# Kernel optimization log

Hardware: AMD Instinct MI355X
Metric: run time of the kernel (lower is better)

The kernel has to match this reference:

```python
import jax, jax.numpy as jnp
import numpy as np

B, T, C, H = 8, 4096, 384, 64

def setup_inputs() -> dict:
    key = jax.random.key(0)
    k1, k2, k3, k4 = jax.random.split(key, 4)
    x = jax.random.normal(k1, (B, T, C), dtype=jnp.float32)
    # nn.Linear(C, H, bias=False) weight applied as x @ W (W stored [C, H])
    s = 1.0 / np.sqrt(C)
    Wk = jax.random.normal(k2, (C, H), dtype=jnp.float32) * s
    Wq = jax.random.normal(k3, (C, H), dtype=jnp.float32) * s
    Wv = jax.random.normal(k4, (C, H), dtype=jnp.float32) * s
    return {"x": x, "Wk": Wk, "Wq": Wq, "Wv": Wv}

def reference(x, Wk, Wq, Wv):
    Bx, Tx, Cx = x.shape
    k = x @ Wk  # [B,T,H]
    q = x @ Wq  # [B,T,H]
    v = x @ Wv  # [B,T,H]
    # NOTE: original scales by C**-0.5 (embedding dim), not head_size**-0.5
    w = jnp.einsum('bth,bsh->bts', q, k) * (Cx ** -0.5)  # [B,T,T]
    causal = jnp.tril(jnp.ones((Tx, Tx), dtype=bool))
    w = jnp.where(causal, w, -jnp.inf)
    w = jax.nn.softmax(w, axis=-1)
    # dropout omitted (eval mode / deterministic reference)
    out = jnp.einsum('bts,bsh->bth', w, v)  # [B,T,H]
    return out
```

## Files before the change

### kernel.cpp

```cpp
#include <hip/hip_runtime.h>
#include <hip/hip_bf16.h>


typedef __bf16 bf16x8 __attribute__((ext_vector_type(8)));
typedef float  f32x4  __attribute__((ext_vector_type(4)));

#define BB   8
#define TT   4096
#define CC   384
#define HH   64
#define NROW (BB*TT)
#define QSCALE (0.05103103630798288f * 1.4426950408889634f)

#if __has_builtin(__builtin_amdgcn_exp2f)
#define EXP2(x) __builtin_amdgcn_exp2f(x)
#else
#define EXP2(x) exp2f(x)
#endif

#define LDS_ROUNDTRIP_FENCE() __asm volatile("s_waitcnt lgkmcnt(0)" ::: "memory")

__device__ __forceinline__ unsigned short f2bf(float f) {
    __bf16 h = (__bf16)f;
    return __builtin_bit_cast(unsigned short, h);
}

__global__ __launch_bounds__(256) void wtrans_kernel(
        const float* __restrict__ Wk,
        const float* __restrict__ Wq,
        const float* __restrict__ Wv,
        unsigned short* __restrict__ Wt) {
    __shared__ __align__(16) unsigned short tile[64][72];
    const float* Wm = (blockIdx.y == 0) ? Wk : ((blockIdx.y == 1) ? Wq : Wv);
    unsigned short* Wtm = Wt + blockIdx.y * (HH * CC);
    const int c0 = blockIdx.x * 64;
#pragma unroll
    for (int i = 0; i < 16; ++i) {
        int id = threadIdx.x + i * 256;
        int c = id >> 6, h = id & 63;
        tile[c][h] = f2bf(Wm[(c0 + c) * HH + h]);
    }
    __syncthreads();
#pragma unroll
    for (int i = 0; i < 16; ++i) {
        int id = threadIdx.x + i * 256;
        int h = id >> 6, c = id & 63;
        Wtm[h * CC + c0 + c] = tile[c][h];
    }
}

__global__ __launch_bounds__(512) void qkv_kernel(
        const float* __restrict__ x,
        const unsigned short* __restrict__ Wt,
        unsigned short* __restrict__ q_ws,
        unsigned short* __restrict__ k_ws,
        unsigned short* __restrict__ vt_ws) {
    __shared__ __align__(16) f32x4 xacc[256 * 13];
    __shared__ __align__(16) unsigned short vtile[64][72];

    const int lane = threadIdx.x & 63;
    const int wv8  = threadIdx.x >> 6;
    const int grp  = wv8 >> 2;
    const int wg   = wv8 & 3;
    const int g256 = threadIdx.x & 255;
    const int l15  = lane & 15;
    const int quad = lane >> 4;
    const int rb   = blockIdx.x * 64;
    const int row  = rb + wg * 16 + l15;

    f32x4 acc[3][4];
    const f32x4 zero = {0.f, 0.f, 0.f, 0.f};
#pragma unroll
    for (int m = 0; m < 3; ++m)
#pragma unroll
        for (int nt = 0; nt < 4; ++nt) acc[m][nt] = zero;

    const float* xrow = x + (long)row * CC + grp * 192;
#pragma unroll
    for (int ch = 0; ch < 3; ++ch) {
#pragma unroll
        for (int kg = 0; kg < 2; ++kg) {
            const int coff = ch * 64 + kg * 32 + quad * 8;
            float4 u0 = *reinterpret_cast<const float4*>(xrow + coff);
            float4 u1 = *reinterpret_cast<const float4*>(xrow + coff + 4);
            bf16x8 a;
            a[0] = (__bf16)u0.x; a[1] = (__bf16)u0.y;
            a[2] = (__bf16)u0.z; a[3] = (__bf16)u0.w;
            a[4] = (__bf16)u1.x; a[5] = (__bf16)u1.y;
            a[6] = (__bf16)u1.z; a[7] = (__bf16)u1.w;
            const int gcoff = grp * 192 + coff;
#pragma unroll
            for (int m = 0; m < 3; ++m) {
                const unsigned short* wtm = Wt + m * (HH * CC);
#pragma unroll
                for (int nt = 0; nt < 4; ++nt) {
                    bf16x8 bfr = *reinterpret_cast<const bf16x8*>(
                        wtm + (nt * 16 + l15) * CC + gcoff);
                    acc[m][nt] = __builtin_amdgcn_mfma_f32_16x16x32_bf16(
                        a, bfr, acc[m][nt], 0, 0, 0);
                }
            }
        }
    }

    const int cidx = g256 * 13;
    if (grp == 1) {
#pragma unroll
        for (int m = 0; m < 3; ++m)
#pragma unroll
            for (int nt = 0; nt < 4; ++nt)
                xacc[cidx + m * 4 + nt] = acc[m][nt];
    }
    __syncthreads();

    if (grp == 0) {
#pragma unroll
        for (int m = 0; m < 3; ++m)
#pragma unroll
            for (int nt = 0; nt < 4; ++nt)
                acc[m][nt] += xacc[cidx + m * 4 + nt];

        const int rt = (rb >> 4) + wg;
#pragma unroll
        for (int nt = 0; nt < 4; ++nt) {
            const int h  = nt * 16 + l15;
            const int c8 = h >> 3;
            const int jj = h & 7;
#pragma unroll
            for (int r = 0; r < 4; ++r) {
                const int gr = rb + wg * 16 + quad * 4 + r;
                const int ii = quad * 4 + r;
                k_ws[((rt * 8 + c8) * 16 + ii) * 8 + jj] = f2bf(acc[0][nt][r]);
                q_ws[gr * HH + h] = f2bf(acc[1][nt][r] * QSCALE);
                vtile[h][ii + wg * 16] = f2bf(acc[2][nt][r]);
            }
        }
    }
    __syncthreads();
    {
        int id = threadIdx.x;
        int dt = id >> 7, sc = (id >> 4) & 7, ii = id & 15;
        unsigned short* dst = vt_ws + (long)(rb >> 6) * 4096
                              + (dt * 8 + sc) * 128 + ii * 8;
        *reinterpret_cast<uint4*>(dst) =
            *reinterpret_cast<const uint4*>(&vtile[dt * 16 + ii][sc * 8]);
    }
}

__global__ __launch_bounds__(1024, 4) void attn_kernel(
        const unsigned short* __restrict__ q_ws,
        const unsigned short* __restrict__ k_ws,
        const unsigned short* __restrict__ vt_ws,
        float* __restrict__ out) {
    __shared__ __align__(16) unsigned short P_lds[16 * 16 * 64];
    __shared__ __align__(16) float xchg[64 * 65];
    __shared__ float mx1[64], lx1[64];

    const int lane = threadIdx.x & 63;
    const int wv16 = threadIdx.x >> 6;
    const int grp  = wv16 >> 2;
    const int wg   = wv16 & 3;
    const int l15  = lane & 15;
    const int quad = lane >> 4;

    const int bid = blockIdx.x;
    const int b   = bid & 7;
    const int qt  = (TT / 64 - 1) - (bid >> 3);
    const int qrow = qt * 64 + wg * 16 + l15;

    const unsigned short* qbase = q_ws + (b * TT + qrow) * HH;
    const bf16x8 qf0 = *reinterpret_cast<const bf16x8*>(qbase + quad * 8);
    const bf16x8 qf1 = *reinterpret_cast<const bf16x8*>(qbase + 32 + quad * 8);

    const f32x4 zero = {0.f, 0.f, 0.f, 0.f};
    f32x4 o[4];
#pragma unroll
    for (int dt = 0; dt < 4; ++dt) o[dt] = zero;
    float mprev = -1e30f, lsum = 0.f;

    const int pbase = wv16 * 1024 + l15 * 64;
    const int pxor  = (l15 & 7) << 3;

    for (int t = grp; t <= qt; t += 4) {
        const int s0 = t * 64;
        const unsigned short* ktile = k_ws + ((long)((b * TT + s0) >> 4)) * 1024;
        const unsigned short* vtile = vt_ws + ((long)((b * TT + s0) >> 6)) * 4096;

        bf16x8 ka0[4], ka1[4];
#pragma unroll
        for (int st = 0; st < 4; ++st) {
            ka0[st] = *reinterpret_cast<const bf16x8*>(
                ktile + ((st * 8 + quad) * 16 + l15) * 8);
            ka1[st] = *reinterpret_cast<const bf16x8*>(
                ktile + ((st * 8 + 4 + quad) * 16 + l15) * 8);
        }
        bf16x8 vb0[4], vb1[4];
#pragma unroll
        for (int dt = 0; dt < 4; ++dt) {
            vb0[dt] = *reinterpret_cast<const bf16x8*>(
                vtile + dt * 1024 + quad * 128 + l15 * 8);
            vb1[dt] = *reinterpret_cast<const bf16x8*>(
                vtile + dt * 1024 + (4 + quad) * 128 + l15 * 8);
        }

        f32x4 sc[4];
#pragma unroll
        for (int st = 0; st < 4; ++st) {
            f32x4 z = zero;
            z = __builtin_amdgcn_mfma_f32_16x16x32_bf16(ka0[st], qf0, z, 0, 0, 0);
            z = __builtin_amdgcn_mfma_f32_16x16x32_bf16(ka1[st], qf1, z, 0, 0, 0);
            sc[st] = z;
        }

        if (t == qt) {
#pragma unroll
            for (int st = 0; st < 4; ++st)
#pragma unroll
                for (int r = 0; r < 4; ++r) {
                    int sg = s0 + st * 16 + quad * 4 + r;
                    if (sg > qrow) sc[st][r] = -1e30f;
                }
        }

        float mloc = -1e30f;
#pragma unroll
        for (int st = 0; st < 4; ++st)
#pragma unroll
            for (int r = 0; r < 4; ++r) mloc = fmaxf(mloc, sc[st][r]);
        mloc = fmaxf(mloc, __shfl_xor(mloc, 16));
        mloc = fmaxf(mloc, __shfl_xor(mloc, 32));
        const float mnew = fmaxf(mprev, mloc);
        const unsigned long long anych = __ballot(mnew > mprev);
        float alpha = 1.0f;
        if (anych) alpha = EXP2(mprev - mnew);

        float psum = 0.f;
#pragma unroll
        for (int st = 0; st < 4; ++st) {
            union { unsigned short us[4]; uint2 u2; } pk;
#pragma unroll
            for (int r = 0; r < 4; ++r) {
                float p = EXP2(sc[st][r] - mnew);
                psum += p;
                pk.us[r] = f2bf(p);
            }
            *reinterpret_cast<uint2*>(
                &P_lds[pbase + ((st * 16 + quad * 4) ^ pxor)]) = pk.u2;
        }
        psum += __shfl_xor(psum, 16);
        psum += __shfl_xor(psum, 32);
        lsum = lsum * alpha + psum;
        mprev = mnew;

        if (anych) {
            float ar[4];
#pragma unroll
            for (int r = 0; r < 4; ++r) ar[r] = __shfl(alpha, quad * 4 + r);
#pragma unroll
            for (int dt = 0; dt < 4; ++dt)
#pragma unroll
                for (int r = 0; r < 4; ++r) o[dt][r] *= ar[r];
        }

        LDS_ROUNDTRIP_FENCE();

        bf16x8 pf0 = *reinterpret_cast<const bf16x8*>(
            &P_lds[pbase + ((quad * 8) ^ pxor)]);
        bf16x8 pf1 = *reinterpret_cast<const bf16x8*>(
            &P_lds[pbase + ((32 + quad * 8) ^ pxor)]);
#pragma unroll
        for (int dt = 0; dt < 4; ++dt) {
            o[dt] = __builtin_amdgcn_mfma_f32_16x16x32_bf16(pf0, vb0[dt], o[dt], 0, 0, 0);
            o[dt] = __builtin_amdgcn_mfma_f32_16x16x32_bf16(pf1, vb1[dt], o[dt], 0, 0, 0);
        }
    }

    for (int rr = 1; rr < 4; ++rr) {
        __syncthreads();
        if (grp == rr) {
            if (quad == 0) { mx1[wg * 16 + l15] = mprev; lx1[wg * 16 + l15] = lsum; }
#pragma unroll
            for (int dt = 0; dt < 4; ++dt)
#pragma unroll
                for (int r = 0; r < 4; ++r)
                    xchg[(wg * 16 + quad * 4 + r) * 65 + dt * 16 + l15] = o[dt][r];
        }
        __syncthreads();
        if (grp == 0) {
#pragma unroll
            for (int r = 0; r < 4; ++r) {
                const int row = wg * 16 + quad * 4 + r;
                const float m0r = __shfl(mprev, quad * 4 + r);
                const float m1r = mx1[row];
                const float ms  = fmaxf(m0r, m1r);
                const float w0  = EXP2(m0r - ms);
                const float w1  = EXP2(m1r - ms);
#pragma unroll
                for (int dt = 0; dt < 4; ++dt)
                    o[dt][r] = o[dt][r] * w0 + xchg[row * 65 + dt * 16 + l15] * w1;
            }
            const float m1l = mx1[wg * 16 + l15];
            const float msl = fmaxf(mprev, m1l);
            lsum = EXP2(mprev - msl) * lsum + EXP2(m1l - msl) * lx1[wg * 16 + l15];
            mprev = msl;
        }
    }

    if (grp == 0) {
        float rl[4];
#pragma unroll
        for (int r = 0; r < 4; ++r) rl[r] = 1.0f / __shfl(lsum, quad * 4 + r);
        const int orow = qt * 64 + wg * 16 + quad * 4;
#pragma unroll
        for (int dt = 0; dt < 4; ++dt)
#pragma unroll
            for (int r = 0; r < 4; ++r)
                out[(long)(b * TT + orow + r) * HH + dt * 16 + l15] = o[dt][r] * rl[r];
    }
}

extern "C" void kernel_launch(void* const* d_in, const int* in_sizes, int n_in,
                              void* d_out, int out_size, void* d_ws, size_t ws_size,
                              hipStream_t stream) {
    const float* x  = (const float*)d_in[0];
    const float* Wk = (const float*)d_in[1];
    const float* Wq = (const float*)d_in[2];
    const float* Wv = (const float*)d_in[3];
    float* out = (float*)d_out;

    char* ws = (char*)d_ws;
    unsigned short* Wt    = (unsigned short*)(ws);
    unsigned short* q_ws  = (unsigned short*)(ws + 147456);
    unsigned short* k_ws  = (unsigned short*)(ws + 147456 + 4194304);
    unsigned short* vt_ws = (unsigned short*)(ws + 147456 + 2 * 4194304);

    wtrans_kernel<<<dim3(6, 3), 256, 0, stream>>>(Wk, Wq, Wv, Wt);
    qkv_kernel<<<NROW / 64, 512, 0, stream>>>(x, Wt, q_ws, k_ws, vt_ws);
    attn_kernel<<<(TT / 64) * BB, 1024, 0, stream>>>(q_ws, k_ws, vt_ws, out);
}
```

Before: 167.5 us.

## Pair causal query tiles per block to balance attention work

Each block now handles two query tiles, a long one (63-p) and a short one (p), so every block does about the same number of key tiles. The grid is halved to 256 blocks. This replaces the previous reverse-order scheduling, which relied on the hardware scheduler to balance the triangular causal workload. In exchange, 256 blocks of 1024 threads may underfill a 256-CU device with lower occupancy, and each block now runs its two tiles serially with an extra merge and barrier.

Measured after the change: 165.8 us. No clear change (-1.0%).

```diff
diff --git a/kernel.cpp b/kernel.cpp
--- a/kernel.cpp
+++ b/kernel.cpp
@@ -165,23 +165,15 @@
 
     const int bid = blockIdx.x;
     const int b   = bid & 7;
-    const int qt  = (TT / 64 - 1) - (bid >> 3);
-    const int qrow = qt * 64 + wg * 16 + l15;
-
-    const unsigned short* qbase = q_ws + (b * TT + qrow) * HH;
-    const bf16x8 qf0 = *reinterpret_cast<const bf16x8*>(qbase + quad * 8);
-    const bf16x8 qf1 = *reinterpret_cast<const bf16x8*>(qbase + 32 + quad * 8);
+    const int p   = bid >> 3;
 
     const f32x4 zero = {0.f, 0.f, 0.f, 0.f};
-    f32x4 o[4];
-#pragma unroll
-    for (int dt = 0; dt < 4; ++dt) o[dt] = zero;
-    float mprev = -1e30f, lsum = 0.f;
-
     const int pbase = wv16 * 1024 + l15 * 64;
     const int pxor  = (l15 & 7) << 3;
 
-    for (int t = grp; t <= qt; t += 4) {
+    auto do_tile = [&](int t, int qt, int qrow,
+                       const bf16x8& qf0, const bf16x8& qf1,
+                       f32x4* o, float& mprev, float& lsum) {
         const int s0 = t * 64;
         const unsigned short* ktile = k_ws + ((long)((b * TT + s0) >> 4)) * 1024;
         const unsigned short* vtile = vt_ws + ((long)((b * TT + s0) >> 6)) * 4096;
@@ -240,9 +232,9 @@
             union { unsigned short us[4]; uint2 u2; } pk;
 #pragma unroll
             for (int r = 0; r < 4; ++r) {
-                float p = EXP2(sc[st][r] - mnew);
-                psum += p;
-                pk.us[r] = f2bf(p);
+                float pv = EXP2(sc[st][r] - mnew);
+                psum += pv;
+                pk.us[r] = f2bf(pv);
             }
             *reinterpret_cast<uint2*>(
                 &P_lds[pbase + ((st * 16 + quad * 4) ^ pxor)]) = pk.u2;
@@ -273,49 +265,81 @@
             o[dt] = __builtin_amdgcn_mfma_f32_16x16x32_bf16(pf0, vb0[dt], o[dt], 0, 0, 0);
             o[dt] = __builtin_amdgcn_mfma_f32_16x16x32_bf16(pf1, vb1[dt], o[dt], 0, 0, 0);
         }
-    }
-
-    for (int rr = 1; rr < 4; ++rr) {
+    };
+
+    auto merge_store = [&](int qt, f32x4* o, float& mprev, float& lsum) {
+        for (int rr = 1; rr < 4; ++rr) {
+            __syncthreads();
+            if (grp == rr) {
+                if (quad == 0) { mx1[wg * 16 + l15] = mprev; lx1[wg * 16 + l15] = lsum; }
+#pragma unroll
+                for (int dt = 0; dt < 4; ++dt)
+#pragma unroll
+                    for (int r = 0; r < 4; ++r)
+                        xchg[(wg * 16 + quad * 4 + r) * 65 + dt * 16 + l15] = o[dt][r];
+            }
+            __syncthreads();
+            if (grp == 0) {
+#pragma unroll
+                for (int r = 0; r < 4; ++r) {
+                    const int row = wg * 16 + quad * 4 + r;
+                    const float m0r = __shfl(mprev, quad * 4 + r);
+                    const float m1r = mx1[row];
+                    const float ms  = fmaxf(m0r, m1r);
+                    const float w0  = EXP2(m0r - ms);
+                    const float w1  = EXP2(m1r - ms);
+#pragma unroll
+                    for (int dt = 0; dt < 4; ++dt)
+                        o[dt][r] = o[dt][r] * w0 + xchg[row * 65 + dt * 16 + l15] * w1;
+                }
+                const float m1l = mx1[wg * 16 + l15];
+                const float msl = fmaxf(mprev, m1l);
+                lsum = EXP2(mprev - msl) * lsum + EXP2(m1l - msl) * lx1[wg * 16 + l15];
+                mprev = msl;
+            }
+        }
+        if (grp == 0) {
+            float rl[4];
+#pragma unroll
+            for (int r = 0; r < 4; ++r) rl[r] = 1.0f / __shfl(lsum, quad * 4 + r);
+            const int orow = qt * 64 + wg * 16 + quad * 4;
+#pragma unroll
+            for (int dt = 0; dt < 4; ++dt)
+#pragma unroll
+                for (int r = 0; r < 4; ++r)
+                    out[(long)(b * TT + orow + r) * HH + dt * 16 + l15] = o[dt][r] * rl[r];
+        }
         __syncthreads();
-        if (grp == rr) {
-            if (quad == 0) { mx1[wg * 16 + l15] = mprev; lx1[wg * 16 + l15] = lsum; }
-#pragma unroll
-            for (int dt = 0; dt < 4; ++dt)
-#pragma unroll
-                for (int r = 0; r < 4; ++r)
-                    xchg[(wg * 16 + quad * 4 + r) * 65 + dt * 16 + l15] = o[dt][r];
-        }
-        __syncthreads();
-        if (grp == 0) {
-#pragma unroll
-            for (int r = 0; r < 4; ++r) {
-                const int row = wg * 16 + quad * 4 + r;
-                const float m0r = __shfl(mprev, quad * 4 + r);
-                const float m1r = mx1[row];
-                const float ms  = fmaxf(m0r, m1r);
-                const float w0  = EXP2(m0r - ms);
-                const float w1  = EXP2(m1r - ms);
-#pragma unroll
-                for (int dt = 0; dt < 4; ++dt)
-                    o[dt][r] = o[dt][r] * w0 + xchg[row * 65 + dt * 16 + l15] * w1;
-            }
-            const float m1l = mx1[wg * 16 + l15];
-            const float msl = fmaxf(mprev, m1l);
-            lsum = EXP2(mprev - msl) * lsum + EXP2(m1l - msl) * lx1[wg * 16 + l15];
-            mprev = msl;
-        }
-    }
-
-    if (grp == 0) {
-        float rl[4];
-#pragma unroll
-        for (int r = 0; r < 4; ++r) rl[r] = 1.0f / __shfl(lsum, quad * 4 + r);
-        const int orow = qt * 64 + wg * 16 + quad * 4;
-#pragma unroll
-        for (int dt = 0; dt < 4; ++dt)
-#pragma unroll
-            for (int r = 0; r < 4; ++r)
-                out[(long)(b * TT + orow + r) * HH + dt * 16 + l15] = o[dt][r] * rl[r];
+    };
+
+    {
+        const int qt = 63 - p;
+        const int qrow = qt * 64 + wg * 16 + l15;
+        const unsigned short* qbase = q_ws + (b * TT + qrow) * HH;
+        const bf16x8 qf0 = *reinterpret_cast<const bf16x8*>(qbase + quad * 8);
+        const bf16x8 qf1 = *reinterpret_cast<const bf16x8*>(qbase + 32 + quad * 8);
+        f32x4 o[4];
+#pragma unroll
+        for (int dt = 0; dt < 4; ++dt) o[dt] = zero;
+        float mprev = -1e30f, lsum = 0.f;
+        for (int t = grp; t <= qt; t += 4)
+            do_tile(t, qt, qrow, qf0, qf1, o, mprev, lsum);
+        merge_store(qt, o, mprev, lsum);
+    }
+
+    {
+        const int qt = p;
+        const int qrow = qt * 64 + wg * 16 + l15;
+        const unsigned short* qbase = q_ws + (b * TT + qrow) * HH;
+        const bf16x8 qf0 = *reinterpret_cast<const bf16x8*>(qbase + quad * 8);
+        const bf16x8 qf1 = *reinterpret_cast<const bf16x8*>(qbase + 32 + quad * 8);
+        f32x4 o[4];
+#pragma unroll
+        for (int dt = 0; dt < 4; ++dt) o[dt] = zero;
+        float mprev = -1e30f, lsum = 0.f;
+        for (int t = grp; t <= qt; t += 4)
+            do_tile(t, qt, qrow, qf0, qf1, o, mprev, lsum);
+        merge_store(qt, o, mprev, lsum);
     }
 }
 
@@ -336,5 +360,5 @@
 
     wtrans_kernel<<<dim3(6, 3), 256, 0, stream>>>(Wk, Wq, Wv, Wt);
     qkv_kernel<<<NROW / 64, 512, 0, stream>>>(x, Wt, q_ws, k_ws, vt_ws);
-    attn_kernel<<<(TT / 64) * BB, 1024, 0, stream>>>(q_ws, k_ws, vt_ws, out);
-}
+    attn_kernel<<<(TT / 128) * BB, 1024, 0, stream>>>(q_ws, k_ws, vt_ws, out);
+}
```
